# Optimization experiments

Hardware: AMD Instinct MI355X
Metric: run time of the kernel (lower is better)

The kernel has to match this reference:

```python
import jax, jax.numpy as jnp
import numpy as np

B, T, C = 16, 4096, 128
CODEBOOK_SIZE = 1024


def setup_inputs() -> dict:
    key = jax.random.key(0)
    kx, ke = jax.random.split(key)
    x = jax.random.normal(kx, (B, T, C), dtype=jnp.float32)
    embed = jax.random.normal(ke, (CODEBOOK_SIZE, C), dtype=jnp.float32)
    return {"x": x, "embed": embed}


def reference(x, embed):
    # x: [B, T, C], embed: [K, C]
    b, t, c = x.shape
    flat = x.reshape(b * t, c)                      # [BT, C]
    # distance = -||x - e||^2, expanded so we never materialize [BT, K, C]
    x_sq = jnp.sum(flat * flat, axis=-1, keepdims=True)   # [BT, 1]
    e_sq = jnp.sum(embed * embed, axis=-1)                 # [K]
    dist = 2.0 * (flat @ embed.T) - x_sq - e_sq[None, :]   # [BT, K]
    embed_ind = jnp.argmax(dist, axis=-1).reshape(b, t)    # [B, T]
    quantized = embed[embed_ind]                           # [B, T, C] gather
    return quantized, embed_ind
```

## Files before the change

### kernel.cpp

```cpp
#include <hip/hip_runtime.h>
#include <float.h>


#define Cdim        128
#define KCODES      1024
#define CH          64
#define NCH         16
#define BROWS       256
#define THREADS     512
#define KK8_OFF     4096
#define IMG_OFF     36864
#define CHUNK_BYTES 32768

typedef _Float16 f16;
typedef __attribute__((ext_vector_type(8)))  _Float16 f16x8;
typedef __attribute__((ext_vector_type(16))) float    f32x16;

__global__ __launch_bounds__(256) void esq_kernel(const float* __restrict__ embed,
                                                  float* __restrict__ esq, int K) {
    int gid  = blockIdx.x * blockDim.x + threadIdx.x;
    int code = gid >> 6;
    int lane = threadIdx.x & 63;
    if (code >= K) return;
    float2 v = ((const float2*)(embed + (size_t)code * Cdim))[lane];
    float  s = fmaf(v.x, v.x, v.y * v.y);
    #pragma unroll
    for (int m = 32; m >= 1; m >>= 1) s += __shfl_xor(s, m, 64);
    if (lane == 0) esq[code] = s;
}

__device__ __forceinline__ void cvt8s(float4 a, float4 b, float scale,
                                      f16x8& h, f16x8& lo) {
    float v[8] = {a.x, a.y, a.z, a.w, b.x, b.y, b.z, b.w};
    #pragma unroll
    for (int i = 0; i < 8; ++i) {
        float s = v[i] * scale;
        f16 hh = (f16)s;
        h[i]  = hh;
        lo[i] = (f16)(s - (float)hh);
    }
}

__global__ __launch_bounds__(256) void bconv_kernel(const float* __restrict__ embed,
                                                    const float* __restrict__ esq,
                                                    char* __restrict__ ws) {
    int t    = blockIdx.x * 256 + threadIdx.x;
    int code = t / 18;
    int slot = t % 18;
    int kk   = slot >> 1;
    int lh   = slot & 1;
    int ch = code >> 6, nt = (code >> 5) & 1, lm = code & 31;
    if (kk < 8) {
        const float4* p = (const float4*)(embed + (size_t)code * Cdim + kk * 16 + lh * 8);
        f16x8 h, lo;
        cvt8s(p[0], p[1], 1.0f, h, lo);
        size_t base = (size_t)IMG_OFF + (size_t)ch * CHUNK_BYTES + nt * 16384
                    + kk * 1024 + lh * 512 + lm * 16;
        *(f16x8*)(ws + base)        = h;
        *(f16x8*)(ws + base + 8192) = lo;
    } else {
        f16x8 f = {};
        if (lh == 0) {
            float e2 = esq[code];
            f16 e2h = (f16)e2;
            f16 e2l = (f16)(e2 - (float)e2h);
            f[0] = -e2h; f[1] = -e2l;
        }
        size_t base = (size_t)KK8_OFF + (size_t)ch * 2048 + nt * 1024
                    + lh * 512 + lm * 16;
        *(f16x8*)(ws + base) = f;
    }
}

__device__ __forceinline__ void gll16(const void* g, void* l) {
    __builtin_amdgcn_global_load_lds(
        (const __attribute__((address_space(1))) unsigned int*)g,
        (__attribute__((address_space(3))) unsigned int*)l, 16, 0, 0);
}

__global__ __launch_bounds__(THREADS) void vq_kernel(
    const float* __restrict__ x, const float* __restrict__ embed,
    const char* __restrict__ ws, float* __restrict__ outq,
    float* __restrict__ outi) {

    __shared__ __align__(16) char  Bb[2][CHUNK_BYTES];
    __shared__ __align__(16) char  Kk8[32768];
    __shared__ float mrg_v[2][BROWS];
    __shared__ int   mrg_i[2][BROWS];
    __shared__ int   winners[BROWS];

    const int tid  = threadIdx.x;
    const int wid  = tid >> 6;
    const int l    = tid & 63;
    const int lm   = l & 31;
    const int lh   = l >> 5;
    const int nt   = wid >> 2;
    const int wr   = wid & 3;
    const int row0 = blockIdx.x * BROWS;
    const int loff = lh * 512 + lm * 16;

    {
        const char* src0 = ws + IMG_OFF + wid * 4096 + (size_t)l * 16;
        char*       dst0 = &Bb[0][wid * 4096];
        #pragma unroll
        for (int i = 0; i < 4; ++i) gll16(src0 + i * 1024, dst0 + i * 1024);
        const char* src1 = ws + KK8_OFF + wid * 4096 + (size_t)l * 16;
        char*       dst1 = Kk8 + wid * 4096;
        #pragma unroll
        for (int i = 0; i < 4; ++i) gll16(src1 + i * 1024, dst1 + i * 1024);
    }

    f16x8 bxh[2][8], bxl[2][8];
    #pragma unroll
    for (int n = 0; n < 2; ++n) {
        const float* xr = x + (size_t)(row0 + wr * 64 + n * 32 + lm) * Cdim + lh * 8;
        #pragma unroll
        for (int kk = 0; kk < 8; ++kk) {
            float4 v0 = *(const float4*)(xr + kk * 16);
            float4 v1 = *(const float4*)(xr + kk * 16 + 4);
            cvt8s(v0, v1, 2.0f, bxh[n][kk], bxl[n][kk]);
        }
    }

    f16x8 bconst = {};
    if (lh == 0) { bconst[0] = (f16)1.f; bconst[1] = (f16)1.f; }

    float best0 = -FLT_MAX, best1 = -FLT_MAX;
    int   bidx0 = 0,        bidx1 = 0;

    asm volatile("s_waitcnt vmcnt(0)" ::: "memory");
    __builtin_amdgcn_s_barrier();

    #pragma unroll 1
    for (int ch = 0; ch < NCH; ++ch) {
        const int cur = ch & 1, nxt = cur ^ 1;

        __builtin_amdgcn_s_barrier();
        if (ch + 1 < NCH) {
            const char* src = ws + IMG_OFF + (size_t)(ch + 1) * CHUNK_BYTES
                            + wid * 4096 + (size_t)l * 16;
            char* dst = &Bb[nxt][wid * 4096];
            #pragma unroll
            for (int i = 0; i < 4; ++i) gll16(src + i * 1024, dst + i * 1024);
            asm volatile("s_waitcnt vmcnt(4)" ::: "memory");
        } else {
            asm volatile("s_waitcnt vmcnt(0)" ::: "memory");
        }
        __builtin_amdgcn_s_barrier();

        f32x16 acc0, acc1;
        #pragma unroll
        for (int r = 0; r < 16; ++r) { acc0[r] = 0.f; acc1[r] = 0.f; }

        const char* bbA = &Bb[cur][nt * 16384 + loff];
        f16x8 ae8 = *(const f16x8*)(&Kk8[ch * 2048 + nt * 1024 + loff]);
        f16x8 aeh = *(const f16x8*)(bbA);
        f16x8 ael = *(const f16x8*)(bbA + 8192);

        #pragma unroll
        for (int kk = 0; kk < 8; ++kk) {
            f16x8 aehN, aelN;
            if (kk < 7) {
                aehN = *(const f16x8*)(bbA + (kk + 1) * 1024);
                aelN = *(const f16x8*)(bbA + 8192 + (kk + 1) * 1024);
            }
            acc0 = __builtin_amdgcn_mfma_f32_32x32x16_f16(aeh, bxh[0][kk], acc0, 0, 0, 0);
            acc1 = __builtin_amdgcn_mfma_f32_32x32x16_f16(aeh, bxh[1][kk], acc1, 0, 0, 0);
            acc0 = __builtin_amdgcn_mfma_f32_32x32x16_f16(ael, bxh[0][kk], acc0, 0, 0, 0);
            acc1 = __builtin_amdgcn_mfma_f32_32x32x16_f16(ael, bxh[1][kk], acc1, 0, 0, 0);
            acc0 = __builtin_amdgcn_mfma_f32_32x32x16_f16(aeh, bxl[0][kk], acc0, 0, 0, 0);
            acc1 = __builtin_amdgcn_mfma_f32_32x32x16_f16(aeh, bxl[1][kk], acc1, 0, 0, 0);
            aeh = aehN; ael = aelN;
        }
        acc0 = __builtin_amdgcn_mfma_f32_32x32x16_f16(ae8, bconst, acc0, 0, 0, 0);
        acc1 = __builtin_amdgcn_mfma_f32_32x32x16_f16(ae8, bconst, acc1, 0, 0, 0);

        const int cb = ch * CH + nt * 32 + lh * 4;
        #pragma unroll
        for (int r = 0; r < 16; ++r) {
            const int code = cb + (r & 3) + 8 * (r >> 2);
            float s0 = acc0[r], s1 = acc1[r];
            if (s0 > best0) { best0 = s0; bidx0 = code; }
            if (s1 > best1) { best1 = s1; bidx1 = code; }
        }
    }

    {
        float v; int vi;
        v = __shfl_xor(best0, 32, 64); vi = __shfl_xor(bidx0, 32, 64);
        if (v > best0 || (v == best0 && vi < bidx0)) { best0 = v; bidx0 = vi; }
        v = __shfl_xor(best1, 32, 64); vi = __shfl_xor(bidx1, 32, 64);
        if (v > best1 || (v == best1 && vi < bidx1)) { best1 = v; bidx1 = vi; }
    }
    if (lh == 0) {
        mrg_v[nt][wr * 64 + lm]      = best0;  mrg_i[nt][wr * 64 + lm]      = bidx0;
        mrg_v[nt][wr * 64 + 32 + lm] = best1;  mrg_i[nt][wr * 64 + 32 + lm] = bidx1;
    }
    __syncthreads();
    if (tid < BROWS) {
        float v0 = mrg_v[0][tid]; int i0 = mrg_i[0][tid];
        float v1 = mrg_v[1][tid]; int i1 = mrg_i[1][tid];
        int bi = (v1 > v0 || (v1 == v0 && i1 < i0)) ? i1 : i0;
        winners[tid] = bi;
        outi[row0 + tid] = (float)bi;
    }
    __syncthreads();

    #pragma unroll
    for (int i = 0; i < 16; ++i) {
        int pos = i * THREADS + tid;
        int r = pos >> 5, c4 = pos & 31;
        int idx = winners[r];
        float4 v = ((const float4*)(embed + (size_t)idx * Cdim))[c4];
        ((float4*)(outq + (size_t)(row0 + r) * Cdim))[c4] = v;
    }
}

extern "C" void kernel_launch(void* const* d_in, const int* in_sizes, int n_in,
                              void* d_out, int out_size, void* d_ws, size_t ws_size,
                              hipStream_t stream) {
    const float* x     = (const float*)d_in[0];
    const float* embed = (const float*)d_in[1];
    const int M = in_sizes[0] / Cdim;
    const int K = in_sizes[1] / Cdim;
    float* outq = (float*)d_out;
    float* outi = outq + (size_t)M * Cdim;

    esq_kernel <<<K / 4, 256, 0, stream>>>(embed, (float*)d_ws, K);
    bconv_kernel<<<72, 256, 0, stream>>>(embed, (const float*)d_ws, (char*)d_ws);
    vq_kernel  <<<M / BROWS, THREADS, 0, stream>>>(x, embed, (const char*)d_ws,
                                                   outq, outi);
}
```

Measured before the change: 68.81 us.

## Halve block size, subtract e_sq from LDS, and software-pipeline MFMA with scoring

Halves rows per block (128 rows, 256 threads) and requests two blocks per CU. Replaces the extra MFMA that folded -||e||^2 into the accumulator with a scalar subtract using e_sq staged in LDS. The chunk loop is restructured so the MFMA for the next chunk is issued before the argmax scoring of the previous one, using two accumulator sets and s_setprio. This aims to hide the scoring VALU work behind matrix ops and improve occupancy, at the cost of more registers and one more barrier-sensitive pipeline stage.

New measurement: 68.90 us. About the same (+0.1%).

```diff
diff --git a/kernel.cpp b/kernel.cpp
--- a/kernel.cpp
+++ b/kernel.cpp
@@ -6,10 +6,9 @@
 #define KCODES      1024
 #define CH          64
 #define NCH         16
-#define BROWS       256
-#define THREADS     512
-#define KK8_OFF     4096
-#define IMG_OFF     36864
+#define BROWS       128
+#define THREADS     256
+#define IMG_OFF     4096
 #define CHUNK_BYTES 32768
 
 typedef _Float16 f16;
@@ -42,34 +41,20 @@
 }
 
 __global__ __launch_bounds__(256) void bconv_kernel(const float* __restrict__ embed,
-                                                    const float* __restrict__ esq,
                                                     char* __restrict__ ws) {
     int t    = blockIdx.x * 256 + threadIdx.x;
-    int code = t / 18;
-    int slot = t % 18;
+    int code = t >> 4;
+    int slot = t & 15;
     int kk   = slot >> 1;
     int lh   = slot & 1;
     int ch = code >> 6, nt = (code >> 5) & 1, lm = code & 31;
-    if (kk < 8) {
-        const float4* p = (const float4*)(embed + (size_t)code * Cdim + kk * 16 + lh * 8);
-        f16x8 h, lo;
-        cvt8s(p[0], p[1], 1.0f, h, lo);
-        size_t base = (size_t)IMG_OFF + (size_t)ch * CHUNK_BYTES + nt * 16384
-                    + kk * 1024 + lh * 512 + lm * 16;
-        *(f16x8*)(ws + base)        = h;
-        *(f16x8*)(ws + base + 8192) = lo;
-    } else {
-        f16x8 f = {};
-        if (lh == 0) {
-            float e2 = esq[code];
-            f16 e2h = (f16)e2;
-            f16 e2l = (f16)(e2 - (float)e2h);
-            f[0] = -e2h; f[1] = -e2l;
-        }
-        size_t base = (size_t)KK8_OFF + (size_t)ch * 2048 + nt * 1024
-                    + lh * 512 + lm * 16;
-        *(f16x8*)(ws + base) = f;
-    }
+    const float4* p = (const float4*)(embed + (size_t)code * Cdim + kk * 16 + lh * 8);
+    f16x8 h, lo;
+    cvt8s(p[0], p[1], 1.0f, h, lo);
+    size_t base = (size_t)IMG_OFF + (size_t)ch * CHUNK_BYTES + nt * 16384
+                + kk * 1024 + lh * 512 + lm * 16;
+    *(f16x8*)(ws + base)        = h;
+    *(f16x8*)(ws + base + 8192) = lo;
 }
 
 __device__ __forceinline__ void gll16(const void* g, void* l) {
@@ -78,13 +63,13 @@
         (__attribute__((address_space(3))) unsigned int*)l, 16, 0, 0);
 }
 
-__global__ __launch_bounds__(THREADS) void vq_kernel(
+__global__ __launch_bounds__(THREADS, 2) void vq_kernel(
     const float* __restrict__ x, const float* __restrict__ embed,
     const char* __restrict__ ws, float* __restrict__ outq,
     float* __restrict__ outi) {
 
     __shared__ __align__(16) char  Bb[2][CHUNK_BYTES];
-    __shared__ __align__(16) char  Kk8[32768];
+    __shared__ __align__(16) float esq_lds[KCODES];
     __shared__ float mrg_v[2][BROWS];
     __shared__ int   mrg_i[2][BROWS];
     __shared__ int   winners[BROWS];
@@ -94,20 +79,17 @@
     const int l    = tid & 63;
     const int lm   = l & 31;
     const int lh   = l >> 5;
-    const int nt   = wid >> 2;
-    const int wr   = wid & 3;
+    const int wr   = wid & 1;
+    const int nt   = wid >> 1;
     const int row0 = blockIdx.x * BROWS;
     const int loff = lh * 512 + lm * 16;
 
     {
-        const char* src0 = ws + IMG_OFF + wid * 4096 + (size_t)l * 16;
-        char*       dst0 = &Bb[0][wid * 4096];
-        #pragma unroll
-        for (int i = 0; i < 4; ++i) gll16(src0 + i * 1024, dst0 + i * 1024);
-        const char* src1 = ws + KK8_OFF + wid * 4096 + (size_t)l * 16;
-        char*       dst1 = Kk8 + wid * 4096;
-        #pragma unroll
-        for (int i = 0; i < 4; ++i) gll16(src1 + i * 1024, dst1 + i * 1024);
+        const char* src = ws + IMG_OFF + wid * 8192 + (size_t)l * 16;
+        char*       dst = &Bb[0][wid * 8192];
+        #pragma unroll
+        for (int i = 0; i < 8; ++i) gll16(src + i * 1024, dst + i * 1024);
+        gll16(ws + wid * 1024 + (size_t)l * 16, (char*)esq_lds + wid * 1024);
     }
 
     f16x8 bxh[2][8], bxl[2][8];
@@ -122,41 +104,31 @@
         }
     }
 
-    f16x8 bconst = {};
-    if (lh == 0) { bconst[0] = (f16)1.f; bconst[1] = (f16)1.f; }
-
     float best0 = -FLT_MAX, best1 = -FLT_MAX;
     int   bidx0 = 0,        bidx1 = 0;
 
-    asm volatile("s_waitcnt vmcnt(0)" ::: "memory");
-    __builtin_amdgcn_s_barrier();
-
-    #pragma unroll 1
-    for (int ch = 0; ch < NCH; ++ch) {
+    auto compute = [&](int ch, f32x16& A0, f32x16& A1) {
         const int cur = ch & 1, nxt = cur ^ 1;
-
         __builtin_amdgcn_s_barrier();
         if (ch + 1 < NCH) {
             const char* src = ws + IMG_OFF + (size_t)(ch + 1) * CHUNK_BYTES
-                            + wid * 4096 + (size_t)l * 16;
-            char* dst = &Bb[nxt][wid * 4096];
+                            + wid * 8192 + (size_t)l * 16;
+            char* dst = &Bb[nxt][wid * 8192];
             #pragma unroll
-            for (int i = 0; i < 4; ++i) gll16(src + i * 1024, dst + i * 1024);
-            asm volatile("s_waitcnt vmcnt(4)" ::: "memory");
+            for (int i = 0; i < 8; ++i) gll16(src + i * 1024, dst + i * 1024);
+            asm volatile("s_waitcnt vmcnt(8)" ::: "memory");
         } else {
             asm volatile("s_waitcnt vmcnt(0)" ::: "memory");
         }
         __builtin_amdgcn_s_barrier();
 
-        f32x16 acc0, acc1;
-        #pragma unroll
-        for (int r = 0; r < 16; ++r) { acc0[r] = 0.f; acc1[r] = 0.f; }
+        #pragma unroll
+        for (int r = 0; r < 16; ++r) { A0[r] = 0.f; A1[r] = 0.f; }
 
         const char* bbA = &Bb[cur][nt * 16384 + loff];
-        f16x8 ae8 = *(const f16x8*)(&Kk8[ch * 2048 + nt * 1024 + loff]);
         f16x8 aeh = *(const f16x8*)(bbA);
         f16x8 ael = *(const f16x8*)(bbA + 8192);
-
+        __builtin_amdgcn_s_setprio(1);
         #pragma unroll
         for (int kk = 0; kk < 8; ++kk) {
             f16x8 aehN, aelN;
@@ -164,26 +136,46 @@
                 aehN = *(const f16x8*)(bbA + (kk + 1) * 1024);
                 aelN = *(const f16x8*)(bbA + 8192 + (kk + 1) * 1024);
             }
-            acc0 = __builtin_amdgcn_mfma_f32_32x32x16_f16(aeh, bxh[0][kk], acc0, 0, 0, 0);
-            acc1 = __builtin_amdgcn_mfma_f32_32x32x16_f16(aeh, bxh[1][kk], acc1, 0, 0, 0);
-            acc0 = __builtin_amdgcn_mfma_f32_32x32x16_f16(ael, bxh[0][kk], acc0, 0, 0, 0);
-            acc1 = __builtin_amdgcn_mfma_f32_32x32x16_f16(ael, bxh[1][kk], acc1, 0, 0, 0);
-            acc0 = __builtin_amdgcn_mfma_f32_32x32x16_f16(aeh, bxl[0][kk], acc0, 0, 0, 0);
-            acc1 = __builtin_amdgcn_mfma_f32_32x32x16_f16(aeh, bxl[1][kk], acc1, 0, 0, 0);
+            A0 = __builtin_amdgcn_mfma_f32_32x32x16_f16(aeh, bxh[0][kk], A0, 0, 0, 0);
+            A1 = __builtin_amdgcn_mfma_f32_32x32x16_f16(aeh, bxh[1][kk], A1, 0, 0, 0);
+            A0 = __builtin_amdgcn_mfma_f32_32x32x16_f16(ael, bxh[0][kk], A0, 0, 0, 0);
+            A1 = __builtin_amdgcn_mfma_f32_32x32x16_f16(ael, bxh[1][kk], A1, 0, 0, 0);
+            A0 = __builtin_amdgcn_mfma_f32_32x32x16_f16(aeh, bxl[0][kk], A0, 0, 0, 0);
+            A1 = __builtin_amdgcn_mfma_f32_32x32x16_f16(aeh, bxl[1][kk], A1, 0, 0, 0);
             aeh = aehN; ael = aelN;
         }
-        acc0 = __builtin_amdgcn_mfma_f32_32x32x16_f16(ae8, bconst, acc0, 0, 0, 0);
-        acc1 = __builtin_amdgcn_mfma_f32_32x32x16_f16(ae8, bconst, acc1, 0, 0, 0);
-
+        __builtin_amdgcn_s_setprio(0);
+    };
+
+    auto score = [&](int ch, const f32x16& A0, const f32x16& A1) {
         const int cb = ch * CH + nt * 32 + lh * 4;
         #pragma unroll
-        for (int r = 0; r < 16; ++r) {
-            const int code = cb + (r & 3) + 8 * (r >> 2);
-            float s0 = acc0[r], s1 = acc1[r];
-            if (s0 > best0) { best0 = s0; bidx0 = code; }
-            if (s1 > best1) { best1 = s1; bidx1 = code; }
-        }
-    }
+        for (int g = 0; g < 4; ++g) {
+            float4 e4 = *(const float4*)&esq_lds[cb + g * 8];
+            #pragma unroll
+            for (int j = 0; j < 4; ++j) {
+                const int r = g * 4 + j;
+                const int code = cb + g * 8 + j;
+                float s0 = A0[r] - ((const float*)&e4)[j];
+                float s1 = A1[r] - ((const float*)&e4)[j];
+                if (s0 > best0) { best0 = s0; bidx0 = code; }
+                if (s1 > best1) { best1 = s1; bidx1 = code; }
+            }
+        }
+    };
+
+    f32x16 aA0, aA1, aB0, aB1;
+    compute(0, aA0, aA1);
+    #pragma unroll 1
+    for (int b = 0; b < 7; ++b) {
+        compute(2 * b + 1, aB0, aB1);
+        score  (2 * b,     aA0, aA1);
+        compute(2 * b + 2, aA0, aA1);
+        score  (2 * b + 1, aB0, aB1);
+    }
+    compute(15, aB0, aB1);
+    score  (14, aA0, aA1);
+    score  (15, aB0, aB1);
 
     {
         float v; int vi;
@@ -227,7 +219,7 @@
     float* outi = outq + (size_t)M * Cdim;
 
     esq_kernel <<<K / 4, 256, 0, stream>>>(embed, (float*)d_ws, K);
-    bconv_kernel<<<72, 256, 0, stream>>>(embed, (const float*)d_ws, (char*)d_ws);
+    bconv_kernel<<<64, 256, 0, stream>>>(embed, (char*)d_ws);
     vq_kernel  <<<M / BROWS, THREADS, 0, stream>>>(x, embed, (const char*)d_ws,
                                                    outq, outi);
 }
```

## Stream codebook tiles from global into registers per wave, drop LDS staging

Applied to the files above, without the earlier changes.

The LDS double buffer and the cross-wave merge go away. Each wave now owns 64 rows and scans all 32 code tiles itself, loading the hi/lo fp16 codebook fragments straight from global (L2) into registers with a two-tile software prefetch. The final argmax is written per wave, and the gather uses readlane broadcasts instead of shared winners. This removes LDS traffic and block-wide synchronisation, but each wave now reads the whole codebook image from cache, which raises L2 traffic and register pressure (launch_bounds 256,1).

After: 71.64 us. +4.1%, slower.

```diff
diff --git a/kernel.cpp b/kernel.cpp
--- a/kernel.cpp
+++ b/kernel.cpp
@@ -2,19 +2,15 @@
 #include <float.h>
 
 
-#define Cdim        128
-#define KCODES      1024
-#define CH          64
-#define NCH         16
-#define BROWS       256
-#define THREADS     512
-#define KK8_OFF     4096
-#define IMG_OFF     36864
-#define CHUNK_BYTES 32768
+#define Cdim    128
+#define KK8_OFF 4096
+#define IMG_OFF 36864
 
 typedef _Float16 f16;
 typedef __attribute__((ext_vector_type(8)))  _Float16 f16x8;
 typedef __attribute__((ext_vector_type(16))) float    f32x16;
+
+#define MFMA(A, B, C) __builtin_amdgcn_mfma_f32_32x32x16_f16((A), (B), (C), 0, 0, 0)
 
 __global__ __launch_bounds__(256) void esq_kernel(const float* __restrict__ embed,
                                                   float* __restrict__ esq, int K) {
@@ -49,13 +45,12 @@
     int slot = t % 18;
     int kk   = slot >> 1;
     int lh   = slot & 1;
-    int ch = code >> 6, nt = (code >> 5) & 1, lm = code & 31;
+    int tile = code >> 5, lm = code & 31;
     if (kk < 8) {
         const float4* p = (const float4*)(embed + (size_t)code * Cdim + kk * 16 + lh * 8);
         f16x8 h, lo;
         cvt8s(p[0], p[1], 1.0f, h, lo);
-        size_t base = (size_t)IMG_OFF + (size_t)ch * CHUNK_BYTES + nt * 16384
-                    + kk * 1024 + lh * 512 + lm * 16;
+        size_t base = (size_t)IMG_OFF + (size_t)tile * 16384 + kk * 1024 + lh * 512 + lm * 16;
         *(f16x8*)(ws + base)        = h;
         *(f16x8*)(ws + base + 8192) = lo;
     } else {
@@ -63,126 +58,96 @@
         if (lh == 0) {
             float e2 = esq[code];
             f16 e2h = (f16)e2;
-            f16 e2l = (f16)(e2 - (float)e2h);
-            f[0] = -e2h; f[1] = -e2l;
+            f[0] = -e2h;
+            f[1] = (f16)-(e2 - (float)e2h);
         }
-        size_t base = (size_t)KK8_OFF + (size_t)ch * 2048 + nt * 1024
-                    + lh * 512 + lm * 16;
-        *(f16x8*)(ws + base) = f;
+        *(f16x8*)(ws + (size_t)KK8_OFF + (size_t)tile * 1024 + lh * 512 + lm * 16) = f;
     }
 }
 
-__device__ __forceinline__ void gll16(const void* g, void* l) {
-    __builtin_amdgcn_global_load_lds(
-        (const __attribute__((address_space(1))) unsigned int*)g,
-        (__attribute__((address_space(3))) unsigned int*)l, 16, 0, 0);
-}
+#define LOADT(T, H, L, E8) do {                                          \
+    const char* _p = img + (size_t)(T) * 16384;                          \
+    _Pragma("unroll")                                                    \
+    for (int _k = 0; _k < 8; ++_k) {                                     \
+        H[_k] = *(const f16x8*)(_p + _k * 1024);                         \
+        L[_k] = *(const f16x8*)(_p + 8192 + _k * 1024);                  \
+    }                                                                    \
+    E8 = *(const f16x8*)(e8p + (size_t)(T) * 1024);                      \
+} while (0)
 
-__global__ __launch_bounds__(THREADS) void vq_kernel(
+#define PROCT(T, H, L, E8) do {                                          \
+    f32x16 _a0, _a1;                                                     \
+    _Pragma("unroll")                                                    \
+    for (int _r = 0; _r < 16; ++_r) { _a0[_r] = 0.f; _a1[_r] = 0.f; }    \
+    _a0 = MFMA(E8, bconst, _a0);                    \
+    _a1 = MFMA(E8, bconst, _a1);                                         \
+    _Pragma("unroll")                                                    \
+    for (int _k = 0; _k < 8; ++_k) {                                     \
+        _a0 = MFMA(H[_k], bxh0[_k], _a0);                                \
+        _a1 = MFMA(H[_k], bxh1[_k], _a1);                                \
+        _a0 = MFMA(L[_k], bxh0[_k], _a0);                                \
+        _a1 = MFMA(L[_k], bxh1[_k], _a1);                                \
+        _a0 = MFMA(H[_k], bxl0[_k], _a0);                                \
+        _a1 = MFMA(H[_k], bxl1[_k], _a1);                                \
+    }                                                                    \
+    const int _cb = (T) * 32 + 4 * lh;                                   \
+    _Pragma("unroll")                                                    \
+    for (int _r = 0; _r < 16; ++_r) {                                    \
+        const int _code = _cb + (_r & 3) + 8 * (_r >> 2);                \
+        float _s0 = _a0[_r], _s1 = _a1[_r];                              \
+        if (_s0 > best0) { best0 = _s0; bidx0 = _code; }                 \
+        if (_s1 > best1) { best1 = _s1; bidx1 = _code; }                 \
+    }                                                                    \
+} while (0)
+
+__global__ __launch_bounds__(256, 1) void vq_kernel(
     const float* __restrict__ x, const float* __restrict__ embed,
     const char* __restrict__ ws, float* __restrict__ outq,
     float* __restrict__ outi) {
-
-    __shared__ __align__(16) char  Bb[2][CHUNK_BYTES];
-    __shared__ __align__(16) char  Kk8[32768];
-    __shared__ float mrg_v[2][BROWS];
-    __shared__ int   mrg_i[2][BROWS];
-    __shared__ int   winners[BROWS];
 
     const int tid  = threadIdx.x;
     const int wid  = tid >> 6;
     const int l    = tid & 63;
     const int lm   = l & 31;
     const int lh   = l >> 5;
-    const int nt   = wid >> 2;
-    const int wr   = wid & 3;
-    const int row0 = blockIdx.x * BROWS;
-    const int loff = lh * 512 + lm * 16;
+    const int wrow = (blockIdx.x * 4 + wid) * 64;
 
+    f16x8 bxh0[8], bxl0[8], bxh1[8], bxl1[8];
     {
-        const char* src0 = ws + IMG_OFF + wid * 4096 + (size_t)l * 16;
-        char*       dst0 = &Bb[0][wid * 4096];
-        #pragma unroll
-        for (int i = 0; i < 4; ++i) gll16(src0 + i * 1024, dst0 + i * 1024);
-        const char* src1 = ws + KK8_OFF + wid * 4096 + (size_t)l * 16;
-        char*       dst1 = Kk8 + wid * 4096;
-        #pragma unroll
-        for (int i = 0; i < 4; ++i) gll16(src1 + i * 1024, dst1 + i * 1024);
-    }
-
-    f16x8 bxh[2][8], bxl[2][8];
-    #pragma unroll
-    for (int n = 0; n < 2; ++n) {
-        const float* xr = x + (size_t)(row0 + wr * 64 + n * 32 + lm) * Cdim + lh * 8;
+        const float* xr0 = x + (size_t)(wrow + lm) * Cdim + lh * 8;
+        const float* xr1 = x + (size_t)(wrow + 32 + lm) * Cdim + lh * 8;
         #pragma unroll
         for (int kk = 0; kk < 8; ++kk) {
-            float4 v0 = *(const float4*)(xr + kk * 16);
-            float4 v1 = *(const float4*)(xr + kk * 16 + 4);
-            cvt8s(v0, v1, 2.0f, bxh[n][kk], bxl[n][kk]);
+            float4 a0 = *(const float4*)(xr0 + kk * 16);
+            float4 a1 = *(const float4*)(xr0 + kk * 16 + 4);
+            cvt8s(a0, a1, 2.0f, bxh0[kk], bxl0[kk]);
+            float4 b0 = *(const float4*)(xr1 + kk * 16);
+            float4 b1 = *(const float4*)(xr1 + kk * 16 + 4);
+            cvt8s(b0, b1, 2.0f, bxh1[kk], bxl1[kk]);
         }
     }
 
     f16x8 bconst = {};
     if (lh == 0) { bconst[0] = (f16)1.f; bconst[1] = (f16)1.f; }
 
+    const char* img = ws + IMG_OFF + (size_t)l * 16;
+    const char* e8p = ws + KK8_OFF + (size_t)l * 16;
+
     float best0 = -FLT_MAX, best1 = -FLT_MAX;
     int   bidx0 = 0,        bidx1 = 0;
 
-    asm volatile("s_waitcnt vmcnt(0)" ::: "memory");
-    __builtin_amdgcn_s_barrier();
+    f16x8 Ah[8], Al[8], Ae8;
+    f16x8 Bh[8], Bl[8], Be8;
+
+    LOADT(0, Ah, Al, Ae8);
 
     #pragma unroll 1
-    for (int ch = 0; ch < NCH; ++ch) {
-        const int cur = ch & 1, nxt = cur ^ 1;
-
+    for (int t = 0; t < 32; t += 2) {
+        LOADT(t + 1, Bh, Bl, Be8);
+        PROCT(t, Ah, Al, Ae8);
+        if (t + 2 < 32) LOADT(t + 2, Ah, Al, Ae8);
+        PROCT(t + 1, Bh, Bl, Be8);
         __builtin_amdgcn_s_barrier();
-        if (ch + 1 < NCH) {
-            const char* src = ws + IMG_OFF + (size_t)(ch + 1) * CHUNK_BYTES
-                            + wid * 4096 + (size_t)l * 16;
-            char* dst = &Bb[nxt][wid * 4096];
-            #pragma unroll
-            for (int i = 0; i < 4; ++i) gll16(src + i * 1024, dst + i * 1024);
-            asm volatile("s_waitcnt vmcnt(4)" ::: "memory");
-        } else {
-            asm volatile("s_waitcnt vmcnt(0)" ::: "memory");
-        }
-        __builtin_amdgcn_s_barrier();
-
-        f32x16 acc0, acc1;
-        #pragma unroll
-        for (int r = 0; r < 16; ++r) { acc0[r] = 0.f; acc1[r] = 0.f; }
-
-        const char* bbA = &Bb[cur][nt * 16384 + loff];
-        f16x8 ae8 = *(const f16x8*)(&Kk8[ch * 2048 + nt * 1024 + loff]);
-        f16x8 aeh = *(const f16x8*)(bbA);
-        f16x8 ael = *(const f16x8*)(bbA + 8192);
-
-        #pragma unroll
-        for (int kk = 0; kk < 8; ++kk) {
-            f16x8 aehN, aelN;
-            if (kk < 7) {
-                aehN = *(const f16x8*)(bbA + (kk + 1) * 1024);
-                aelN = *(const f16x8*)(bbA + 8192 + (kk + 1) * 1024);
-            }
-            acc0 = __builtin_amdgcn_mfma_f32_32x32x16_f16(aeh, bxh[0][kk], acc0, 0, 0, 0);
-            acc1 = __builtin_amdgcn_mfma_f32_32x32x16_f16(aeh, bxh[1][kk], acc1, 0, 0, 0);
-            acc0 = __builtin_amdgcn_mfma_f32_32x32x16_f16(ael, bxh[0][kk], acc0, 0, 0, 0);
-            acc1 = __builtin_amdgcn_mfma_f32_32x32x16_f16(ael, bxh[1][kk], acc1, 0, 0, 0);
-            acc0 = __builtin_amdgcn_mfma_f32_32x32x16_f16(aeh, bxl[0][kk], acc0, 0, 0, 0);
-            acc1 = __builtin_amdgcn_mfma_f32_32x32x16_f16(aeh, bxl[1][kk], acc1, 0, 0, 0);
-            aeh = aehN; ael = aelN;
-        }
-        acc0 = __builtin_amdgcn_mfma_f32_32x32x16_f16(ae8, bconst, acc0, 0, 0, 0);
-        acc1 = __builtin_amdgcn_mfma_f32_32x32x16_f16(ae8, bconst, acc1, 0, 0, 0);
-
-        const int cb = ch * CH + nt * 32 + lh * 4;
-        #pragma unroll
-        for (int r = 0; r < 16; ++r) {
-            const int code = cb + (r & 3) + 8 * (r >> 2);
-            float s0 = acc0[r], s1 = acc1[r];
-            if (s0 > best0) { best0 = s0; bidx0 = code; }
-            if (s1 > best1) { best1 = s1; bidx1 = code; }
-        }
     }
 
     {
@@ -192,27 +157,20 @@
         v = __shfl_xor(best1, 32, 64); vi = __shfl_xor(bidx1, 32, 64);
         if (v > best1 || (v == best1 && vi < bidx1)) { best1 = v; bidx1 = vi; }
     }
+
     if (lh == 0) {
-        mrg_v[nt][wr * 64 + lm]      = best0;  mrg_i[nt][wr * 64 + lm]      = bidx0;
-        mrg_v[nt][wr * 64 + 32 + lm] = best1;  mrg_i[nt][wr * 64 + 32 + lm] = bidx1;
+        outi[wrow + lm]      = (float)bidx0;
+        outi[wrow + 32 + lm] = (float)bidx1;
     }
-    __syncthreads();
-    if (tid < BROWS) {
-        float v0 = mrg_v[0][tid]; int i0 = mrg_i[0][tid];
-        float v1 = mrg_v[1][tid]; int i1 = mrg_i[1][tid];
-        int bi = (v1 > v0 || (v1 == v0 && i1 < i0)) ? i1 : i0;
-        winners[tid] = bi;
-        outi[row0 + tid] = (float)bi;
-    }
-    __syncthreads();
 
     #pragma unroll
-    for (int i = 0; i < 16; ++i) {
-        int pos = i * THREADS + tid;
-        int r = pos >> 5, c4 = pos & 31;
-        int idx = winners[r];
-        float4 v = ((const float4*)(embed + (size_t)idx * Cdim))[c4];
-        ((float4*)(outq + (size_t)(row0 + r) * Cdim))[c4] = v;
+    for (int r = 0; r < 32; ++r) {
+        int i0 = __builtin_amdgcn_readlane(bidx0, r);
+        int i1 = __builtin_amdgcn_readlane(bidx1, r);
+        float2 v0 = ((const float2*)(embed + (size_t)i0 * Cdim))[l];
+        float2 v1 = ((const float2*)(embed + (size_t)i1 * Cdim))[l];
+        ((float2*)(outq + (size_t)(wrow + r) * Cdim))[l]      = v0;
+        ((float2*)(outq + (size_t)(wrow + 32 + r) * Cdim))[l] = v1;
     }
 }
 
@@ -228,6 +186,6 @@
 
     esq_kernel <<<K / 4, 256, 0, stream>>>(embed, (float*)d_ws, K);
     bconv_kernel<<<72, 256, 0, stream>>>(embed, (const float*)d_ws, (char*)d_ws);
-    vq_kernel  <<<M / BROWS, THREADS, 0, stream>>>(x, embed, (const char*)d_ws,
-                                                   outq, outi);
+    vq_kernel  <<<M / 256, 256, 0, stream>>>(x, embed, (const char*)d_ws,
+                                             outq, outi);
 }
```
